# Optimization experiments

Hardware: AMD Instinct MI355X
Metric: run time of the kernel (lower is better)

The kernel has to match this reference:

```python
import jax, jax.numpy as jnp
import numpy as np

B, T, C, H = 4, 2048, 1024, 16
D = C // H  # head dim = 64


def setup_inputs() -> dict:
    key = jax.random.key(0)
    ks = jax.random.split(key, 5)
    s = 0.02
    return {
        "x": jax.random.normal(ks[0], (B, T, C), dtype=jnp.float32),
        "W_attn": jax.random.normal(ks[1], (C, 3 * C), dtype=jnp.float32) * s,
        "b_attn": jnp.zeros((3 * C,), dtype=jnp.float32),
        "W_proj": jax.random.normal(ks[2], (C, C), dtype=jnp.float32) * s,
        "b_proj": jnp.zeros((C,), dtype=jnp.float32),
    }


def reference(x, W_attn, b_attn, W_proj, b_proj):
    # qkv projection: [B,T,3C]
    qkv = x @ W_attn + b_attn
    q, k, v = jnp.split(qkv, 3, axis=-1)
    # [B,T,C] -> [B,H,T,D]
    def heads(t):
        return t.reshape(B, T, H, D).transpose(0, 2, 1, 3)
    q, k, v = heads(q), heads(k), heads(v)
    # scaled scores with causal mask, materialized [B,H,T,T] as in original
    att = jnp.einsum('bhqd,bhkd->bhqk', q, k) * (1.0 / np.sqrt(D))
    causal = jnp.tril(jnp.ones((T, T), dtype=bool))
    att = jnp.where(causal[None, None], att, -jnp.inf)
    att = jax.nn.softmax(att, axis=-1)
    y = jnp.einsum('bhqk,bhkd->bhqd', att, v)  # [B,H,T,D]
    y = y.transpose(0, 2, 1, 3).reshape(B, T, C)
    y = y @ W_proj + b_proj
    # original also returns present=(k,v); it is a pure pass-through cache
    return y
```

## Files before the change

kernel.cpp:

```cpp
#include <hip/hip_runtime.h>


typedef unsigned short u16;
typedef unsigned int u32;
typedef __attribute__((ext_vector_type(8))) unsigned short u16x8;
typedef __attribute__((ext_vector_type(4))) unsigned short u16x4;
typedef __attribute__((ext_vector_type(8))) short short8;
typedef __attribute__((ext_vector_type(4))) float f32x4;

__device__ inline u16 f2bf(float f) {
  unsigned u = __float_as_uint(f);
  u = (u + 0x7FFF + ((u >> 16) & 1)) >> 16;
  return (u16)u;
}

__device__ inline f32x4 mfma16(short8 a, short8 b, f32x4 c) {
  return __builtin_amdgcn_mfma_f32_16x16x32_bf16(a, b, c, 0, 0, 0);
}

__device__ inline void gld16(const void* g, void* l) {
  __builtin_amdgcn_global_load_lds(
      (const __attribute__((address_space(1))) void*)g,
      (__attribute__((address_space(3))) void*)l, 16, 0, 0);
}

__global__ __launch_bounds__(256) void k_cvt(const float* __restrict__ in,
                                             u16* __restrict__ out) {
  int i = (blockIdx.x * 256 + threadIdx.x) * 4;
  float4 v = *(const float4*)(in + i);
  u16x4 o = {f2bf(v.x), f2bf(v.y), f2bf(v.z), f2bf(v.w)};
  *(u16x4*)(out + i) = o;
}

__global__ __launch_bounds__(256) void k_tw(const float* __restrict__ in,
                                            u16* __restrict__ outT, int R, int Cc) {
  __shared__ u16 t[64][65];
  int c0 = blockIdx.x * 64, r0 = blockIdx.y * 64;
  int a = threadIdx.x & 63, w = threadIdx.x >> 6;
#pragma unroll
  for (int j = 0; j < 16; ++j) {
    int r = w + j * 4;
    t[r][a] = f2bf(in[(size_t)(r0 + r) * Cc + c0 + a]);
  }
  __syncthreads();
#pragma unroll
  for (int j = 0; j < 16; ++j) {
    int c = w + j * 4;
    outT[(size_t)(c0 + c) * R + r0 + a] = t[a][c];
  }
}

__global__ __launch_bounds__(256) void k_tv(const u16* __restrict__ qkv,
                                            u16* __restrict__ vt) {
  __shared__ u16 t[64][65];
  int t0 = blockIdx.x * 64, h = blockIdx.y, b = blockIdx.z;
  int a = threadIdx.x & 63, w = threadIdx.x >> 6;
#pragma unroll
  for (int j = 0; j < 16; ++j) {
    int tr = w + j * 4;
    t[tr][a] = qkv[(size_t)(b * 2048 + t0 + tr) * 3072 + 2048 + h * 64 + a];
  }
  __syncthreads();
#pragma unroll
  for (int j = 0; j < 16; ++j) {
    int d = w + j * 4;
    vt[((size_t)((b * 16 + h) * 64 + d)) * 2048 + t0 + a] = t[a][d];
  }
}

template <int OUTBF, int QSCALE>
__global__ __launch_bounds__(256) void gemm_bt(const u16* __restrict__ A,
                                               const u16* __restrict__ Bt,
                                               const float* __restrict__ bias,
                                               u16* __restrict__ outb,
                                               float* __restrict__ outf,
                                               int M, int N, int K) {
  __shared__ u16 As[128 * 32];
  __shared__ u16 Bs[128 * 32];
  const int m0 = blockIdx.x * 128, n0 = blockIdx.y * 128;
  const int tid = threadIdx.x, wave = tid >> 6, lane = tid & 63;
  const int quad = lane >> 4, l16 = lane & 15;
  const int wm = wave & 1, wn = wave >> 1;
  f32x4 acc[4][4] = {};
  for (int kt = 0; kt < K; kt += 32) {
    __syncthreads();
#pragma unroll
    for (int j = 0; j < 2; ++j) {
      int c = wave * 128 + j * 64 + lane;
      int row = c >> 2, col = (c & 3) * 8;
      gld16(A + (size_t)(m0 + row) * K + kt + col, As + (size_t)(wave * 128 + j * 64) * 8);
      gld16(Bt + (size_t)(n0 + row) * K + kt + col, Bs + (size_t)(wave * 128 + j * 64) * 8);
    }
    __syncthreads();
    short8 af[4], bf[4];
#pragma unroll
    for (int mt = 0; mt < 4; ++mt)
      af[mt] = *(const short8*)(As + (wm * 64 + mt * 16 + l16) * 32 + quad * 8);
#pragma unroll
    for (int nt = 0; nt < 4; ++nt)
      bf[nt] = *(const short8*)(Bs + (wn * 64 + nt * 16 + l16) * 32 + quad * 8);
#pragma unroll
    for (int mt = 0; mt < 4; ++mt)
#pragma unroll
      for (int nt = 0; nt < 4; ++nt)
        acc[mt][nt] = mfma16(af[mt], bf[nt], acc[mt][nt]);
  }
#pragma unroll
  for (int nt = 0; nt < 4; ++nt) {
    int col = n0 + wn * 64 + nt * 16 + l16;
    float bv = bias[col];
#pragma unroll
    for (int mt = 0; mt < 4; ++mt) {
      int rowb = m0 + wm * 64 + mt * 16 + quad * 4;
#pragma unroll
      for (int r = 0; r < 4; ++r) {
        float v = acc[mt][nt][r] + bv;
        if (QSCALE && col < 1024) v *= 0.18033688f;
        if (OUTBF)
          outb[(size_t)(rowb + r) * N + col] = f2bf(v);
        else
          outf[(size_t)(rowb + r) * N + col] = v;
      }
    }
  }
}

#define ATP 72
__global__ __launch_bounds__(256) void attn(const u16* __restrict__ qkv,
                                            const u16* __restrict__ vt,
                                            u16* __restrict__ y) {
  __shared__ u16 shm[256 * ATP];
  u16* Qs = shm;
  u16* Ks = shm + 128 * ATP;
  u16* Vs = shm + 192 * ATP;
  const int p = blockIdx.x, h = blockIdx.y, b = blockIdx.z;
  const int tid = threadIdx.x, wave = tid >> 6, lane = tid & 63;
  const int quad = lane >> 4, l16 = lane & 15;
  const u16* Qg = qkv + (size_t)b * 2048 * 3072 + h * 64;
  const u16* Kg = Qg + 1024;
  const u16* Vtg = vt + (size_t)(b * 16 + h) * 64 * 2048;
  const int srow0 = tid >> 3, scol0 = (tid & 7) * 8;
  u16* Pw0 = Qs + (wave * 16) * ATP;
  u16* Pw1 = Qs + (64 + wave * 16) * ATP;
  short8 ones_f;
#pragma unroll
  for (int j = 0; j < 8; ++j) ones_f[j] = 0x3F80;

  for (int half = 0; half < 2; ++half) {
    const int qb = half ? (15 - p) : p;
    const int q0 = qb * 128;
    const int nkt = 2 * qb + 2;
    const u16* kp0 = Kg + (size_t)srow0 * 3072 + scol0;
    const u16* kp1 = kp0 + 32 * 3072;
    const u16* vp0 = Vtg + (size_t)srow0 * 2048 + scol0;
    const u16* vp1 = vp0 + 32 * 2048;
    u16x8 qr0 = *(const u16x8*)(Qg + (size_t)(q0 + srow0) * 3072 + scol0);
    u16x8 qr1 = *(const u16x8*)(Qg + (size_t)(q0 + srow0 + 32) * 3072 + scol0);
    u16x8 qr2 = *(const u16x8*)(Qg + (size_t)(q0 + srow0 + 64) * 3072 + scol0);
    u16x8 qr3 = *(const u16x8*)(Qg + (size_t)(q0 + srow0 + 96) * 3072 + scol0);
    u16x8 kreg0 = *(const u16x8*)kp0, kreg1 = *(const u16x8*)kp1;
    u16x8 vreg0 = *(const u16x8*)vp0, vreg1 = *(const u16x8*)vp1;
    __syncthreads();
    *(u16x8*)&Qs[(size_t)srow0 * ATP + scol0] = qr0;
    *(u16x8*)&Qs[(size_t)(srow0 + 32) * ATP + scol0] = qr1;
    *(u16x8*)&Qs[(size_t)(srow0 + 64) * ATP + scol0] = qr2;
    *(u16x8*)&Qs[(size_t)(srow0 + 96) * ATP + scol0] = qr3;
    *(u16x8*)&Ks[(size_t)srow0 * ATP + scol0] = kreg0;
    *(u16x8*)&Ks[(size_t)(srow0 + 32) * ATP + scol0] = kreg1;
    *(u16x8*)&Vs[(size_t)srow0 * ATP + scol0] = vreg0;
    *(u16x8*)&Vs[(size_t)(srow0 + 32) * ATP + scol0] = vreg1;
    __syncthreads();
    short8 qf0a = *(const short8*)&Qs[(wave * 16 + l16) * ATP + quad * 8];
    short8 qf1a = *(const short8*)&Qs[(wave * 16 + l16) * ATP + 32 + quad * 8];
    short8 qf0b = *(const short8*)&Qs[(64 + wave * 16 + l16) * ATP + quad * 8];
    short8 qf1b = *(const short8*)&Qs[(64 + wave * 16 + l16) * ATP + 32 + quad * 8];

    f32x4 lacc0 = {}, lacc1 = {};
    f32x4 o0[4] = {}, o1[4] = {};

    auto tile = [&](int kt, int g0mode, bool g1mask) {
      if (kt > 0) {
        __syncthreads();
        *(u16x8*)&Ks[(size_t)srow0 * ATP + scol0] = kreg0;
        *(u16x8*)&Ks[(size_t)(srow0 + 32) * ATP + scol0] = kreg1;
        *(u16x8*)&Vs[(size_t)srow0 * ATP + scol0] = vreg0;
        *(u16x8*)&Vs[(size_t)(srow0 + 32) * ATP + scol0] = vreg1;
        __syncthreads();
      }
      if (kt + 1 < nkt) {
        kreg0 = *(const u16x8*)(kp0 += 64 * 3072);
        kreg1 = *(const u16x8*)(kp1 += 64 * 3072);
        vreg0 = *(const u16x8*)(vp0 += 64);
        vreg1 = *(const u16x8*)(vp1 += 64);
      }

      f32x4 s0[4] = {}, s1[4] = {};
#pragma unroll
      for (int mt = 0; mt < 4; ++mt) {
        short8 kf0 = *(const short8*)&Ks[(mt * 16 + l16) * ATP + quad * 8];
        short8 kf1 = *(const short8*)&Ks[(mt * 16 + l16) * ATP + 32 + quad * 8];
        if (g0mode < 2) {
          s0[mt] = mfma16(kf0, qf0a, s0[mt]);
          s0[mt] = mfma16(kf1, qf1a, s0[mt]);
        }
        s1[mt] = mfma16(kf0, qf0b, s1[mt]);
        s1[mt] = mfma16(kf1, qf1b, s1[mt]);
      }

      if (g0mode < 2) {
        const int qrow = q0 + wave * 16 + l16;
#pragma unroll
        for (int mt = 0; mt < 4; ++mt) {
          float pe[4];
#pragma unroll
          for (int r = 0; r < 4; ++r) {
            float pv = __builtin_amdgcn_exp2f(s0[mt][r]);
            if (g0mode == 1) {
              int kcol = kt * 64 + mt * 16 + quad * 4 + r;
              if (kcol > qrow) pv = 0.f;
            }
            pe[r] = pv;
          }
          u32 lo = __builtin_amdgcn_perm(__float_as_uint(pe[1]),
                                         __float_as_uint(pe[0]), 0x07060302u);
          u32 hi = __builtin_amdgcn_perm(__float_as_uint(pe[3]),
                                         __float_as_uint(pe[2]), 0x07060302u);
          uint2 pk = {lo, hi};
          *(uint2*)&Pw0[l16 * ATP + mt * 16 + quad * 4] = pk;
        }
      }
      {
        const int qrow = q0 + 64 + wave * 16 + l16;
#pragma unroll
        for (int mt = 0; mt < 4; ++mt) {
          float pe[4];
#pragma unroll
          for (int r = 0; r < 4; ++r) {
            float pv = __builtin_amdgcn_exp2f(s1[mt][r]);
            if (g1mask) {
              int kcol = kt * 64 + mt * 16 + quad * 4 + r;
              if (kcol > qrow) pv = 0.f;
            }
            pe[r] = pv;
          }
          u32 lo = __builtin_amdgcn_perm(__float_as_uint(pe[1]),
                                         __float_as_uint(pe[0]), 0x07060302u);
          u32 hi = __builtin_amdgcn_perm(__float_as_uint(pe[3]),
                                         __float_as_uint(pe[2]), 0x07060302u);
          uint2 pk = {lo, hi};
          *(uint2*)&Pw1[l16 * ATP + mt * 16 + quad * 4] = pk;
        }
      }

#pragma unroll
      for (int ks = 0; ks < 2; ++ks) {
        short8 pf0, pf1;
        if (g0mode < 2) {
          pf0 = *(const short8*)&Pw0[l16 * ATP + ks * 32 + quad * 8];
          lacc0 = mfma16(pf0, ones_f, lacc0);
        }
        pf1 = *(const short8*)&Pw1[l16 * ATP + ks * 32 + quad * 8];
        lacc1 = mfma16(pf1, ones_f, lacc1);
#pragma unroll
        for (int dt = 0; dt < 4; ++dt) {
          short8 vf = *(const short8*)&Vs[(dt * 16 + l16) * ATP + ks * 32 + quad * 8];
          if (g0mode < 2) o0[dt] = mfma16(pf0, vf, o0[dt]);
          o1[dt] = mfma16(pf1, vf, o1[dt]);
        }
      }
    };

    for (int kt = 0; kt < nkt - 2; ++kt) tile(kt, 0, false);
    tile(nkt - 2, 1, false);
    tile(nkt - 1, 2, true);

    size_t rb0 = (size_t)b * 2048 + q0 + wave * 16 + quad * 4;
#pragma unroll
    for (int r = 0; r < 4; ++r) {
      float inv = 1.f / lacc0[r];
#pragma unroll
      for (int dt = 0; dt < 4; ++dt)
        y[(rb0 + r) * 1024 + h * 64 + dt * 16 + l16] = f2bf(o0[dt][r] * inv);
    }
    size_t rb1 = rb0 + 64;
#pragma unroll
    for (int r = 0; r < 4; ++r) {
      float inv = 1.f / lacc1[r];
#pragma unroll
      for (int dt = 0; dt < 4; ++dt)
        y[(rb1 + r) * 1024 + h * 64 + dt * 16 + l16] = f2bf(o1[dt][r] * inv);
    }
  }
}

extern "C" void kernel_launch(void* const* d_in, const int* in_sizes, int n_in,
                              void* d_out, int out_size, void* d_ws, size_t ws_size,
                              hipStream_t stream) {
  const float* x = (const float*)d_in[0];
  const float* W_attn = (const float*)d_in[1];
  const float* b_attn = (const float*)d_in[2];
  const float* W_proj = (const float*)d_in[3];
  const float* b_proj = (const float*)d_in[4];
  float* out = (float*)d_out;
  char* ws = (char*)d_ws;
  u16* xb  = (u16*)(ws);
  u16* wta = (u16*)(ws + 16777216);
  u16* wtp = (u16*)(ws + 23068672);
  u16* qkv = (u16*)(ws + 25165824);
  u16* vt  = (u16*)(ws + 75497472);
  u16* y   = (u16*)(ws + 92274688);

  k_cvt<<<dim3(8192), 256, 0, stream>>>(x, xb);
  k_tw<<<dim3(48, 16), 256, 0, stream>>>(W_attn, wta, 1024, 3072);
  k_tw<<<dim3(16, 16), 256, 0, stream>>>(W_proj, wtp, 1024, 1024);
  gemm_bt<1, 1><<<dim3(64, 24), 256, 0, stream>>>(xb, wta, b_attn, qkv, nullptr, 8192, 3072, 1024);
  k_tv<<<dim3(32, 16, 4), 256, 0, stream>>>(qkv, vt);
  attn<<<dim3(8, 16, 4), 256, 0, stream>>>(qkv, vt, y);
  gemm_bt<0, 0><<<dim3(64, 8), 256, 0, stream>>>(y, wtp, b_proj, nullptr, out, 8192, 1024, 1024);
}
```

Before: 264.2 us.

## Enlarge GEMM tile to 256x128 with XOR-swizzled LDS and hoisted pointers

The bf16 GEMM tile grows from 128x128 to 256x128, so each wave computes 128x64 with 8x4 MFMA accumulators. This raises arithmetic intensity per LDS load. LDS chunk placement is XOR-swizzled to cut bank conflicts on the fragment reads, and global load addresses are precomputed outside the k loop. The costs are roughly double the accumulator registers (hence launch_bounds 256,2) and half as many blocks: 768 for the QKV GEMM and only 256 for the projection GEMM, which can leave CUs underused.

```diff
diff --git a/kernel.cpp b/kernel.cpp
--- a/kernel.cpp
+++ b/kernel.cpp
@@ -69,49 +69,63 @@
 }
 
 template <int OUTBF, int QSCALE>
-__global__ __launch_bounds__(256) void gemm_bt(const u16* __restrict__ A,
-                                               const u16* __restrict__ Bt,
-                                               const float* __restrict__ bias,
-                                               u16* __restrict__ outb,
-                                               float* __restrict__ outf,
-                                               int M, int N, int K) {
-  __shared__ u16 As[128 * 32];
+__global__ __launch_bounds__(256, 2) void gemm_bt(const u16* __restrict__ A,
+                                                  const u16* __restrict__ Bt,
+                                                  const float* __restrict__ bias,
+                                                  u16* __restrict__ outb,
+                                                  float* __restrict__ outf,
+                                                  int M, int N, int K) {
+  __shared__ u16 As[256 * 32];
   __shared__ u16 Bs[128 * 32];
-  const int m0 = blockIdx.x * 128, n0 = blockIdx.y * 128;
+  const int m0 = blockIdx.x * 256, n0 = blockIdx.y * 128;
   const int tid = threadIdx.x, wave = tid >> 6, lane = tid & 63;
   const int quad = lane >> 4, l16 = lane & 15;
-  const int wm = wave & 1, wn = wave >> 1;
-  f32x4 acc[4][4] = {};
+  const int wm = (wave >> 1) * 128, wn = (wave & 1) * 64;
+  const int sw = (l16 >> 1) & 3;
+  const int gch = (lane & 3) ^ ((lane >> 3) & 3);
+  const int lrow = lane >> 2;
+  const u16* pa0 = A + (size_t)(m0 + wave * 64 + 0 + lrow) * K + gch * 8;
+  const u16* pa1 = A + (size_t)(m0 + wave * 64 + 16 + lrow) * K + gch * 8;
+  const u16* pa2 = A + (size_t)(m0 + wave * 64 + 32 + lrow) * K + gch * 8;
+  const u16* pa3 = A + (size_t)(m0 + wave * 64 + 48 + lrow) * K + gch * 8;
+  const u16* pb0 = Bt + (size_t)(n0 + wave * 32 + 0 + lrow) * K + gch * 8;
+  const u16* pb1 = Bt + (size_t)(n0 + wave * 32 + 16 + lrow) * K + gch * 8;
+  u16* la0 = As + (wave * 256 + 0) * 8;
+  u16* la1 = As + (wave * 256 + 64) * 8;
+  u16* la2 = As + (wave * 256 + 128) * 8;
+  u16* la3 = As + (wave * 256 + 192) * 8;
+  u16* lb0 = Bs + (wave * 128 + 0) * 8;
+  u16* lb1 = Bs + (wave * 128 + 64) * 8;
+  f32x4 acc[8][4] = {};
   for (int kt = 0; kt < K; kt += 32) {
     __syncthreads();
-#pragma unroll
-    for (int j = 0; j < 2; ++j) {
-      int c = wave * 128 + j * 64 + lane;
-      int row = c >> 2, col = (c & 3) * 8;
-      gld16(A + (size_t)(m0 + row) * K + kt + col, As + (size_t)(wave * 128 + j * 64) * 8);
-      gld16(Bt + (size_t)(n0 + row) * K + kt + col, Bs + (size_t)(wave * 128 + j * 64) * 8);
-    }
+    gld16(pa0 + kt, la0);
+    gld16(pa1 + kt, la1);
+    gld16(pa2 + kt, la2);
+    gld16(pa3 + kt, la3);
+    gld16(pb0 + kt, lb0);
+    gld16(pb1 + kt, lb1);
     __syncthreads();
-    short8 af[4], bf[4];
-#pragma unroll
-    for (int mt = 0; mt < 4; ++mt)
-      af[mt] = *(const short8*)(As + (wm * 64 + mt * 16 + l16) * 32 + quad * 8);
+    short8 af[8], bf[4];
+#pragma unroll
+    for (int mt = 0; mt < 8; ++mt)
+      af[mt] = *(const short8*)(As + (wm + mt * 16 + l16) * 32 + (quad ^ sw) * 8);
 #pragma unroll
     for (int nt = 0; nt < 4; ++nt)
-      bf[nt] = *(const short8*)(Bs + (wn * 64 + nt * 16 + l16) * 32 + quad * 8);
-#pragma unroll
-    for (int mt = 0; mt < 4; ++mt)
+      bf[nt] = *(const short8*)(Bs + (wn + nt * 16 + l16) * 32 + (quad ^ sw) * 8);
+#pragma unroll
+    for (int mt = 0; mt < 8; ++mt)
 #pragma unroll
       for (int nt = 0; nt < 4; ++nt)
         acc[mt][nt] = mfma16(af[mt], bf[nt], acc[mt][nt]);
   }
 #pragma unroll
   for (int nt = 0; nt < 4; ++nt) {
-    int col = n0 + wn * 64 + nt * 16 + l16;
+    int col = n0 + wn + nt * 16 + l16;
     float bv = bias[col];
 #pragma unroll
-    for (int mt = 0; mt < 4; ++mt) {
-      int rowb = m0 + wm * 64 + mt * 16 + quad * 4;
+    for (int mt = 0; mt < 8; ++mt) {
+      int rowb = m0 + wm + mt * 16 + quad * 4;
 #pragma unroll
       for (int r = 0; r < 4; ++r) {
         float v = acc[mt][nt][r] + bv;
@@ -313,8 +327,8 @@
   k_cvt<<<dim3(8192), 256, 0, stream>>>(x, xb);
   k_tw<<<dim3(48, 16), 256, 0, stream>>>(W_attn, wta, 1024, 3072);
   k_tw<<<dim3(16, 16), 256, 0, stream>>>(W_proj, wtp, 1024, 1024);
-  gemm_bt<1, 1><<<dim3(64, 24), 256, 0, stream>>>(xb, wta, b_attn, qkv, nullptr, 8192, 3072, 1024);
+  gemm_bt<1, 1><<<dim3(32, 24), 256, 0, stream>>>(xb, wta, b_attn, qkv, nullptr, 8192, 3072, 1024);
   k_tv<<<dim3(32, 16, 4), 256, 0, stream>>>(qkv, vt);
   attn<<<dim3(8, 16, 4), 256, 0, stream>>>(qkv, vt, y);
-  gemm_bt<0, 0><<<dim3(64, 8), 256, 0, stream>>>(y, wtp, b_proj, nullptr, out, 8192, 1024, 1024);
-}
+  gemm_bt<0, 0><<<dim3(32, 8), 256, 0, stream>>>(y, wtp, b_proj, nullptr, out, 8192, 1024, 1024);
+}
```

New measurement: 279.1 us. 1.06x slower.

## Double GEMM K-tile to 64 with XOR-swizzled LDS layout and precomputed load addresses

Applied to the files above, without the earlier changes.

Raises the GEMM K step from 32 to 64, so each tile iteration does twice the MFMA work per pair of barriers. The global-to-LDS loads now place 16-byte chunks in an XOR-swizzled order keyed on the row, and the fragment reads apply the matching swizzle to avoid LDS bank conflicts with the wider 64-element rows. Source and destination pointers are computed once before the loop instead of on every iteration. LDS use per block doubles, which may limit occupancy.

```diff
diff --git a/kernel.cpp b/kernel.cpp
--- a/kernel.cpp
+++ b/kernel.cpp
@@ -75,43 +75,61 @@
                                                u16* __restrict__ outb,
                                                float* __restrict__ outf,
                                                int M, int N, int K) {
-  __shared__ u16 As[128 * 32];
-  __shared__ u16 Bs[128 * 32];
+  __shared__ u16 As[128 * 64];
+  __shared__ u16 Bs[128 * 64];
   const int m0 = blockIdx.x * 128, n0 = blockIdx.y * 128;
   const int tid = threadIdx.x, wave = tid >> 6, lane = tid & 63;
   const int quad = lane >> 4, l16 = lane & 15;
-  const int wm = wave & 1, wn = wave >> 1;
+  const int wm = (wave & 1) * 64, wn = (wave >> 1) * 64;
+  const int lrow = lane >> 3;
+  const int gch = (lane & 7) ^ lrow;
+  const u16* sA[4];
+  const u16* sB[4];
+  u16* dA[4];
+  u16* dB[4];
+#pragma unroll
+  for (int j = 0; j < 4; ++j) {
+    int r = wave * 32 + j * 8;
+    sA[j] = A + (size_t)(m0 + r + lrow) * K + gch * 8;
+    sB[j] = Bt + (size_t)(n0 + r + lrow) * K + gch * 8;
+    dA[j] = As + r * 64;
+    dB[j] = Bs + r * 64;
+  }
   f32x4 acc[4][4] = {};
-  for (int kt = 0; kt < K; kt += 32) {
+  for (int kt = 0; kt < K; kt += 64) {
     __syncthreads();
 #pragma unroll
-    for (int j = 0; j < 2; ++j) {
-      int c = wave * 128 + j * 64 + lane;
-      int row = c >> 2, col = (c & 3) * 8;
-      gld16(A + (size_t)(m0 + row) * K + kt + col, As + (size_t)(wave * 128 + j * 64) * 8);
-      gld16(Bt + (size_t)(n0 + row) * K + kt + col, Bs + (size_t)(wave * 128 + j * 64) * 8);
+    for (int j = 0; j < 4; ++j) {
+      gld16(sA[j] + kt, dA[j]);
+      gld16(sB[j] + kt, dB[j]);
     }
     __syncthreads();
-    short8 af[4], bf[4];
-#pragma unroll
-    for (int mt = 0; mt < 4; ++mt)
-      af[mt] = *(const short8*)(As + (wm * 64 + mt * 16 + l16) * 32 + quad * 8);
-#pragma unroll
-    for (int nt = 0; nt < 4; ++nt)
-      bf[nt] = *(const short8*)(Bs + (wn * 64 + nt * 16 + l16) * 32 + quad * 8);
-#pragma unroll
-    for (int mt = 0; mt < 4; ++mt)
+#pragma unroll
+    for (int ks = 0; ks < 2; ++ks) {
+      const int sl = l16 & 7;
+      short8 af[4], bf[4];
+#pragma unroll
+      for (int mt = 0; mt < 4; ++mt)
+        af[mt] = *(const short8*)(As + (wm + mt * 16 + l16) * 64 +
+                                  (((ks * 4 + quad) ^ sl)) * 8);
 #pragma unroll
       for (int nt = 0; nt < 4; ++nt)
-        acc[mt][nt] = mfma16(af[mt], bf[nt], acc[mt][nt]);
+        bf[nt] = *(const short8*)(Bs + (wn + nt * 16 + l16) * 64 +
+                                  (((ks * 4 + quad) ^ sl)) * 8);
+#pragma unroll
+      for (int mt = 0; mt < 4; ++mt)
+#pragma unroll
+        for (int nt = 0; nt < 4; ++nt)
+          acc[mt][nt] = mfma16(af[mt], bf[nt], acc[mt][nt]);
+    }
   }
 #pragma unroll
   for (int nt = 0; nt < 4; ++nt) {
-    int col = n0 + wn * 64 + nt * 16 + l16;
+    int col = n0 + wn + nt * 16 + l16;
     float bv = bias[col];
 #pragma unroll
     for (int mt = 0; mt < 4; ++mt) {
-      int rowb = m0 + wm * 64 + mt * 16 + quad * 4;
+      int rowb = m0 + wm + mt * 16 + quad * 4;
 #pragma unroll
       for (int r = 0; r < 4; ++r) {
         float v = acc[mt][nt][r] + bv;
```

Result: faster. 254.2 us (-3.8%).
